# Optimization experiments

Hardware: AMD Instinct MI355X
Metric: run time of the kernel (lower is better)

## Reference

```python
import jax, jax.numpy as jnp
import numpy as np

N_NODES = 50000
N_EDGES = 800000
D = 64  # out_dim


def setup_inputs() -> dict:
    key = jax.random.key(0)
    ks = jax.random.split(key, 9)
    K_h = jax.random.normal(ks[0], (N_NODES, D), dtype=jnp.float32)
    Q_h = jax.random.normal(ks[1], (N_NODES, D), dtype=jnp.float32)
    P_e = jax.random.normal(ks[2], (N_NODES, D), dtype=jnp.float32)
    src = jax.random.randint(ks[3], (N_EDGES,), 0, N_NODES, dtype=jnp.int32)
    dst = jax.random.randint(ks[4], (N_EDGES,), 0, N_NODES, dtype=jnp.int32)
    # MLP params: Linear(D, D) -> ReLU -> Linear(D, 1)
    lim1 = 1.0 / np.sqrt(D)
    W1 = jax.random.uniform(ks[5], (D, D), minval=-lim1, maxval=lim1, dtype=jnp.float32)
    b1 = jax.random.uniform(ks[6], (D,), minval=-lim1, maxval=lim1, dtype=jnp.float32)
    W2 = jax.random.uniform(ks[7], (D, 1), minval=-lim1, maxval=lim1, dtype=jnp.float32)
    b2 = jax.random.uniform(ks[8], (1,), minval=-lim1, maxval=lim1, dtype=jnp.float32)
    return {"K_h": K_h, "Q_h": Q_h, "P_e": P_e, "src": src, "dst": dst,
            "W1": W1, "b1": b1, "W2": W2, "b2": b2}


def reference(K_h, Q_h, P_e, src, dst, W1, b1, W2, b2):
    # Per-edge gather: src node K_h and P_e, dst node Q_h -> [E, D]
    dif = K_h[src] - Q_h[dst] + P_e[src]
    # Tiny 2-layer MLP per edge: [E, D] -> [E, D] -> [E, 1]
    h = jax.nn.relu(dif @ W1 + b1)
    score = h @ W2 + b2  # [E, 1]
    return score
```

## Files before the change

### kernel.cpp

```cpp
#include <hip/hip_runtime.h>
#include <hip/hip_fp16.h>

#define DD 64
#define NPB 64
#define LP 72

typedef _Float16 f16x8 __attribute__((ext_vector_type(8)));
typedef float    f32x4 __attribute__((ext_vector_type(4)));

__global__ __launch_bounds__(256) void node_transform_mfma(
    const float* __restrict__ K_h, const float* __restrict__ Q_h,
    const float* __restrict__ P_e, const float* __restrict__ W1,
    const float* __restrict__ b1, __half* __restrict__ A,
    __half* __restrict__ Bm, int n_nodes)
{
    __shared__ __half XH [NPB][LP];
    __shared__ __half QH [NPB][LP];
    __shared__ __half W1T[DD][LP];

    const int tid   = threadIdx.x;
    const int nbase = blockIdx.x * NPB;

    {
        const int k  = tid >> 2;
        const int n0 = (tid & 3) << 4;
        const float* wr = W1 + k * DD + n0;
        float4 w0 = *(const float4*)(wr);
        float4 w1v = *(const float4*)(wr + 4);
        float4 w2v = *(const float4*)(wr + 8);
        float4 w3v = *(const float4*)(wr + 12);
        const float wv[16] = {w0.x,w0.y,w0.z,w0.w, w1v.x,w1v.y,w1v.z,w1v.w,
                              w2v.x,w2v.y,w2v.z,w2v.w, w3v.x,w3v.y,w3v.z,w3v.w};
#pragma unroll
        for (int j = 0; j < 16; ++j)
            W1T[n0 + j][k] = __float2half(wv[j]);
    }

#pragma unroll
    for (int ch = 0; ch < 4; ++ch) {
        int idx = tid + (ch << 8);
        int r   = idx >> 4;
        int q4  = idx & 15;
        int node = nbase + r;
        float4 kv = make_float4(0.f,0.f,0.f,0.f);
        float4 pv = kv, qv = kv;
        if (node < n_nodes) {
            kv = *(const float4*)(K_h + (size_t)node * DD + q4 * 4);
            pv = *(const float4*)(P_e + (size_t)node * DD + q4 * 4);
            qv = *(const float4*)(Q_h + (size_t)node * DD + q4 * 4);
        }
        __half2* xh = (__half2*)&XH[r][q4 << 2];
        xh[0] = __float22half2_rn(make_float2(kv.x + pv.x, kv.y + pv.y));
        xh[1] = __float22half2_rn(make_float2(kv.z + pv.z, kv.w + pv.w));
        __half2* qh = (__half2*)&QH[r][q4 << 2];
        qh[0] = __float22half2_rn(make_float2(qv.x, qv.y));
        qh[1] = __float22half2_rn(make_float2(qv.z, qv.w));
    }
    __syncthreads();

    const int w    = tid >> 6;
    const int lane = tid & 63;
    const int m    = lane & 15;
    const int q    = lane >> 4;
    const int row  = (w << 4) + m;

    f16x8 xlo = *(const f16x8*)&XH[row][(q << 3)];
    f16x8 xhi = *(const f16x8*)&XH[row][32 + (q << 3)];
    f16x8 qlo = *(const f16x8*)&QH[row][(q << 3)];
    f16x8 qhi = *(const f16x8*)&QH[row][32 + (q << 3)];

    f32x4 accA[4], accB[4];
#pragma unroll
    for (int t = 0; t < 4; ++t) {
        float bb = b1[t * 16 + m];
        accA[t] = (f32x4){bb, bb, bb, bb};
        accB[t] = (f32x4){0.f, 0.f, 0.f, 0.f};
        f16x8 wlo = *(const f16x8*)&W1T[t * 16 + m][(q << 3)];
        f16x8 whi = *(const f16x8*)&W1T[t * 16 + m][32 + (q << 3)];
        accA[t] = __builtin_amdgcn_mfma_f32_16x16x32_f16(xlo, wlo, accA[t], 0, 0, 0);
        accA[t] = __builtin_amdgcn_mfma_f32_16x16x32_f16(xhi, whi, accA[t], 0, 0, 0);
        accB[t] = __builtin_amdgcn_mfma_f32_16x16x32_f16(qlo, wlo, accB[t], 0, 0, 0);
        accB[t] = __builtin_amdgcn_mfma_f32_16x16x32_f16(qhi, whi, accB[t], 0, 0, 0);
    }

#pragma unroll
    for (int r = 0; r < 4; ++r) {
        int node = nbase + (w << 4) + (q << 2) + r;
        if (node >= n_nodes) continue;
        __half* Arow = A  + (size_t)node * DD + m;
        __half* Brow = Bm + (size_t)node * DD + m;
#pragma unroll
        for (int t = 0; t < 4; ++t) {
            Arow[t * 16] = __float2half(accA[t][r]);
            Brow[t * 16] = __float2half(accB[t][r]);
        }
    }
}

__global__ __launch_bounds__(256) void edge_score_kernel(
    const __half* __restrict__ A, const __half* __restrict__ Bm,
    const int* __restrict__ src, const int* __restrict__ dst,
    const float* __restrict__ W2, const float* __restrict__ b2,
    float* __restrict__ out, int n_edges)
{
    const int tid = threadIdx.x;
    const int g   = tid >> 3;
    const int c   = tid & 7;
    const int e0  = (blockIdx.x << 7) + (g << 2);
    if (e0 >= n_edges) return;

    float4 w0 = *(const float4*)(W2 + c * 8);
    float4 w1 = *(const float4*)(W2 + c * 8 + 4);
    const float wv[8] = {w0.x, w0.y, w0.z, w0.w, w1.x, w1.y, w1.z, w1.w};
    const size_t coff = (size_t)(c * 8);

    if (e0 + 3 < n_edges) {
        int4 sv = *(const int4*)(src + e0);
        int4 dv = *(const int4*)(dst + e0);

        float4 ra0 = *(const float4*)(A  + (size_t)sv.x * DD + coff);
        float4 rb0 = *(const float4*)(Bm + (size_t)dv.x * DD + coff);
        float4 ra1 = *(const float4*)(A  + (size_t)sv.y * DD + coff);
        float4 rb1 = *(const float4*)(Bm + (size_t)dv.y * DD + coff);
        float4 ra2 = *(const float4*)(A  + (size_t)sv.z * DD + coff);
        float4 rb2 = *(const float4*)(Bm + (size_t)dv.z * DD + coff);
        float4 ra3 = *(const float4*)(A  + (size_t)sv.w * DD + coff);
        float4 rb3 = *(const float4*)(Bm + (size_t)dv.w * DD + coff);

        float acc0 = 0.f, acc1 = 0.f, acc2 = 0.f, acc3 = 0.f;
        const __half2* ah0 = (const __half2*)&ra0;
        const __half2* bh0 = (const __half2*)&rb0;
        const __half2* ah1 = (const __half2*)&ra1;
        const __half2* bh1 = (const __half2*)&rb1;
        const __half2* ah2 = (const __half2*)&ra2;
        const __half2* bh2 = (const __half2*)&rb2;
        const __half2* ah3 = (const __half2*)&ra3;
        const __half2* bh3 = (const __half2*)&rb3;
#pragma unroll
        for (int j = 0; j < 4; ++j) {
            float2 x, y;
            x = __half22float2(ah0[j]); y = __half22float2(bh0[j]);
            acc0 = fmaf(fmaxf(x.x - y.x, 0.f), wv[2 * j + 0], acc0);
            acc0 = fmaf(fmaxf(x.y - y.y, 0.f), wv[2 * j + 1], acc0);
            x = __half22float2(ah1[j]); y = __half22float2(bh1[j]);
            acc1 = fmaf(fmaxf(x.x - y.x, 0.f), wv[2 * j + 0], acc1);
            acc1 = fmaf(fmaxf(x.y - y.y, 0.f), wv[2 * j + 1], acc1);
            x = __half22float2(ah2[j]); y = __half22float2(bh2[j]);
            acc2 = fmaf(fmaxf(x.x - y.x, 0.f), wv[2 * j + 0], acc2);
            acc2 = fmaf(fmaxf(x.y - y.y, 0.f), wv[2 * j + 1], acc2);
            x = __half22float2(ah3[j]); y = __half22float2(bh3[j]);
            acc3 = fmaf(fmaxf(x.x - y.x, 0.f), wv[2 * j + 0], acc3);
            acc3 = fmaf(fmaxf(x.y - y.y, 0.f), wv[2 * j + 1], acc3);
        }

        acc0 += __shfl_xor(acc0, 1); acc1 += __shfl_xor(acc1, 1);
        acc2 += __shfl_xor(acc2, 1); acc3 += __shfl_xor(acc3, 1);
        acc0 += __shfl_xor(acc0, 2); acc1 += __shfl_xor(acc1, 2);
        acc2 += __shfl_xor(acc2, 2); acc3 += __shfl_xor(acc3, 2);
        acc0 += __shfl_xor(acc0, 4); acc1 += __shfl_xor(acc1, 4);
        acc2 += __shfl_xor(acc2, 4); acc3 += __shfl_xor(acc3, 4);

        if (c == 0) {
            float bb = b2[0];
            *(float4*)(out + e0) =
                make_float4(acc0 + bb, acc1 + bb, acc2 + bb, acc3 + bb);
        }
    } else {
        for (int e = e0; e < n_edges && e < e0 + 4; ++e) {
            int s = src[e], d = dst[e];
            float4 ar = *(const float4*)(A  + (size_t)s * DD + coff);
            float4 br = *(const float4*)(Bm + (size_t)d * DD + coff);
            const __half2* ah = (const __half2*)&ar;
            const __half2* bh = (const __half2*)&br;
            float acc = 0.f;
#pragma unroll
            for (int j = 0; j < 4; ++j) {
                float2 x = __half22float2(ah[j]);
                float2 y = __half22float2(bh[j]);
                acc = fmaf(fmaxf(x.x - y.x, 0.f), wv[2 * j + 0], acc);
                acc = fmaf(fmaxf(x.y - y.y, 0.f), wv[2 * j + 1], acc);
            }
            acc += __shfl_xor(acc, 1);
            acc += __shfl_xor(acc, 2);
            acc += __shfl_xor(acc, 4);
            if (c == 0) out[e] = acc + b2[0];
        }
    }
}

extern "C" void kernel_launch(void* const* d_in, const int* in_sizes, int n_in,
                              void* d_out, int out_size, void* d_ws, size_t ws_size,
                              hipStream_t stream) {
    const float* K_h = (const float*)d_in[0];
    const float* Q_h = (const float*)d_in[1];
    const float* P_e = (const float*)d_in[2];
    const int*   src = (const int*)d_in[3];
    const int*   dst = (const int*)d_in[4];
    const float* W1  = (const float*)d_in[5];
    const float* b1  = (const float*)d_in[6];
    const float* W2  = (const float*)d_in[7];
    const float* b2  = (const float*)d_in[8];
    float* out = (float*)d_out;

    int n_nodes = in_sizes[0] / DD;
    int n_edges = in_sizes[3];

    __half* A  = (__half*)d_ws;
    __half* Bm = A + (size_t)n_nodes * DD;

    node_transform_mfma<<<(n_nodes + NPB - 1) / NPB, 256, 0, stream>>>(
        K_h, Q_h, P_e, W1, b1, A, Bm, n_nodes);
    edge_score_kernel<<<(n_edges + 127) / 128, 256, 0, stream>>>(
        A, Bm, src, dst, W2, b2, out, n_edges);
}
```

Before: 120.9 us.

## Bin edges by source node range before gathering to improve locality

Adds a histogram, scan and scatter pass that groups edges into coarse bins by src node index, then runs the edge scoring kernel over the reordered (src,dst) pairs and scatters each result back to its original edge slot. The aim is to make the A-row gathers hit nearby memory so they get more cache reuse. In exchange it adds three extra kernel launches, an extra pass over the src/dst arrays with shared-memory atomics, and an uncoalesced scatter of the output. The binning is rebuilt from scratch on every call.

```diff
diff --git a/kernel.cpp b/kernel.cpp
--- a/kernel.cpp
+++ b/kernel.cpp
@@ -4,6 +4,7 @@
 #define DD 64
 #define NPB 64
 #define LP 72
+#define MAXB 512
 
 typedef _Float16 f16x8 __attribute__((ext_vector_type(8)));
 typedef float    f32x4 __attribute__((ext_vector_type(4)));
@@ -12,7 +13,7 @@
     const float* __restrict__ K_h, const float* __restrict__ Q_h,
     const float* __restrict__ P_e, const float* __restrict__ W1,
     const float* __restrict__ b1, __half* __restrict__ A,
-    __half* __restrict__ Bm, int n_nodes)
+    __half* __restrict__ Bm, int n_nodes, int* __restrict__ counts)
 {
     __shared__ __half XH [NPB][LP];
     __shared__ __half QH [NPB][LP];
@@ -20,6 +21,10 @@
 
     const int tid   = threadIdx.x;
     const int nbase = blockIdx.x * NPB;
+
+    if (blockIdx.x == 0) {
+        for (int i = tid; i < MAXB; i += 256) counts[i] = 0;
+    }
 
     {
         const int k  = tid >> 2;
@@ -97,9 +102,78 @@
     }
 }
 
-__global__ __launch_bounds__(256) void edge_score_kernel(
+
+__global__ __launch_bounds__(256) void hist_kernel(
+    const int* __restrict__ src, int* __restrict__ counts,
+    int n_edges, int shift)
+{
+    __shared__ int lh[MAXB];
+    for (int i = threadIdx.x; i < MAXB; i += 256) lh[i] = 0;
+    __syncthreads();
+    int idx    = blockIdx.x * blockDim.x + threadIdx.x;
+    int stride = gridDim.x * blockDim.x;
+    for (int e = idx; e < n_edges; e += stride)
+        atomicAdd(&lh[src[e] >> shift], 1);
+    __syncthreads();
+    for (int i = threadIdx.x; i < MAXB; i += 256)
+        if (lh[i]) atomicAdd(&counts[i], lh[i]);
+}
+
+__global__ __launch_bounds__(MAXB) void scan_kernel(
+    const int* __restrict__ counts, int* __restrict__ cursors, int nb)
+{
+    __shared__ int buf[2][MAXB];
+    const int t = threadIdx.x;
+    int v = (t < nb) ? counts[t] : 0;
+    buf[0][t] = v;
+    __syncthreads();
+    int s = 0;
+#pragma unroll
+    for (int off = 1; off < MAXB; off <<= 1) {
+        int x = buf[s][t];
+        if (t >= off) x += buf[s][t - off];
+        buf[s ^ 1][t] = x;
+        s ^= 1;
+        __syncthreads();
+    }
+    if (t < nb) cursors[t] = buf[s][t] - v;
+}
+
+__global__ __launch_bounds__(256) void scatter_kernel(
+    const int* __restrict__ src, const int* __restrict__ dst,
+    int* __restrict__ cursors, int2* __restrict__ sd, int* __restrict__ eid,
+    int n_edges, int shift)
+{
+    __shared__ int lh[MAXB];
+    __shared__ int base[MAXB];
+    const int t     = threadIdx.x;
+    const int chunk = (n_edges + gridDim.x - 1) / gridDim.x;
+    const int e0    = blockIdx.x * chunk;
+    const int e1    = (e0 + chunk < n_edges) ? e0 + chunk : n_edges;
+
+    for (int i = t; i < MAXB; i += 256) lh[i] = 0;
+    __syncthreads();
+    for (int e = e0 + t; e < e1; e += 256)
+        atomicAdd(&lh[src[e] >> shift], 1);
+    __syncthreads();
+    for (int i = t; i < MAXB; i += 256) {
+        int c = lh[i];
+        base[i] = c ? atomicAdd(&cursors[i], c) : 0;
+        lh[i] = 0;
+    }
+    __syncthreads();
+    for (int e = e0 + t; e < e1; e += 256) {
+        int sv = src[e];
+        int b  = sv >> shift;
+        int pos = base[b] + atomicAdd(&lh[b], 1);
+        sd[pos]  = make_int2(sv, dst[e]);
+        eid[pos] = e;
+    }
+}
+
+__global__ __launch_bounds__(256) void edge_score_binned(
     const __half* __restrict__ A, const __half* __restrict__ Bm,
-    const int* __restrict__ src, const int* __restrict__ dst,
+    const int2* __restrict__ sd, const int* __restrict__ eid,
     const float* __restrict__ W2, const float* __restrict__ b2,
     float* __restrict__ out, int n_edges)
 {
@@ -115,17 +189,18 @@
     const size_t coff = (size_t)(c * 8);
 
     if (e0 + 3 < n_edges) {
-        int4 sv = *(const int4*)(src + e0);
-        int4 dv = *(const int4*)(dst + e0);
-
-        float4 ra0 = *(const float4*)(A  + (size_t)sv.x * DD + coff);
-        float4 rb0 = *(const float4*)(Bm + (size_t)dv.x * DD + coff);
-        float4 ra1 = *(const float4*)(A  + (size_t)sv.y * DD + coff);
-        float4 rb1 = *(const float4*)(Bm + (size_t)dv.y * DD + coff);
-        float4 ra2 = *(const float4*)(A  + (size_t)sv.z * DD + coff);
-        float4 rb2 = *(const float4*)(Bm + (size_t)dv.z * DD + coff);
-        float4 ra3 = *(const float4*)(A  + (size_t)sv.w * DD + coff);
-        float4 rb3 = *(const float4*)(Bm + (size_t)dv.w * DD + coff);
+        int4 p01 = *(const int4*)(sd + e0);
+        int4 p23 = *(const int4*)(sd + e0 + 2);
+        int4 ev  = *(const int4*)(eid + e0);
+
+        float4 ra0 = *(const float4*)(A  + (size_t)p01.x * DD + coff);
+        float4 rb0 = *(const float4*)(Bm + (size_t)p01.y * DD + coff);
+        float4 ra1 = *(const float4*)(A  + (size_t)p01.z * DD + coff);
+        float4 rb1 = *(const float4*)(Bm + (size_t)p01.w * DD + coff);
+        float4 ra2 = *(const float4*)(A  + (size_t)p23.x * DD + coff);
+        float4 rb2 = *(const float4*)(Bm + (size_t)p23.y * DD + coff);
+        float4 ra3 = *(const float4*)(A  + (size_t)p23.z * DD + coff);
+        float4 rb3 = *(const float4*)(Bm + (size_t)p23.w * DD + coff);
 
         float acc0 = 0.f, acc1 = 0.f, acc2 = 0.f, acc3 = 0.f;
         const __half2* ah0 = (const __half2*)&ra0;
@@ -162,14 +237,16 @@
 
         if (c == 0) {
             float bb = b2[0];
-            *(float4*)(out + e0) =
-                make_float4(acc0 + bb, acc1 + bb, acc2 + bb, acc3 + bb);
+            out[ev.x] = acc0 + bb;
+            out[ev.y] = acc1 + bb;
+            out[ev.z] = acc2 + bb;
+            out[ev.w] = acc3 + bb;
         }
     } else {
         for (int e = e0; e < n_edges && e < e0 + 4; ++e) {
-            int s = src[e], d = dst[e];
-            float4 ar = *(const float4*)(A  + (size_t)s * DD + coff);
-            float4 br = *(const float4*)(Bm + (size_t)d * DD + coff);
+            int2 p = sd[e];
+            float4 ar = *(const float4*)(A  + (size_t)p.x * DD + coff);
+            float4 br = *(const float4*)(Bm + (size_t)p.y * DD + coff);
             const __half2* ah = (const __half2*)&ar;
             const __half2* bh = (const __half2*)&br;
             float acc = 0.f;
@@ -183,7 +260,7 @@
             acc += __shfl_xor(acc, 1);
             acc += __shfl_xor(acc, 2);
             acc += __shfl_xor(acc, 4);
-            if (c == 0) out[e] = acc + b2[0];
+            if (c == 0) out[eid[e]] = acc + b2[0];
         }
     }
 }
@@ -205,11 +282,28 @@
     int n_nodes = in_sizes[0] / DD;
     int n_edges = in_sizes[3];
 
+    int shift = 7;
+    while ((((n_nodes - 1) >> shift) + 1) > MAXB) ++shift;
+    int nb = ((n_nodes - 1) >> shift) + 1;
+
+    size_t nA = (size_t)n_nodes * DD;
     __half* A  = (__half*)d_ws;
-    __half* Bm = A + (size_t)n_nodes * DD;
+    __half* Bm = A + nA;
+    char* p = (char*)(Bm + nA);
+    p = (char*)(((size_t)p + 255) & ~(size_t)255);
+    int2* sd = (int2*)p;   p += (size_t)n_edges * sizeof(int2);
+    p = (char*)(((size_t)p + 255) & ~(size_t)255);
+    int* eid = (int*)p;    p += (size_t)n_edges * sizeof(int);
+    p = (char*)(((size_t)p + 255) & ~(size_t)255);
+    int* counts  = (int*)p;  p += MAXB * sizeof(int);
+    int* cursors = (int*)p;
 
     node_transform_mfma<<<(n_nodes + NPB - 1) / NPB, 256, 0, stream>>>(
-        K_h, Q_h, P_e, W1, b1, A, Bm, n_nodes);
-    edge_score_kernel<<<(n_edges + 127) / 128, 256, 0, stream>>>(
-        A, Bm, src, dst, W2, b2, out, n_edges);
-}
+        K_h, Q_h, P_e, W1, b1, A, Bm, n_nodes, counts);
+    hist_kernel<<<256, 256, 0, stream>>>(src, counts, n_edges, shift);
+    scan_kernel<<<1, MAXB, 0, stream>>>(counts, cursors, nb);
+    scatter_kernel<<<256, 256, 0, stream>>>(src, dst, cursors, sd, eid,
+                                            n_edges, shift);
+    edge_score_binned<<<(n_edges + 127) / 128, 256, 0, stream>>>(
+        A, Bm, sd, eid, W2, b2, out, n_edges);
+}
```

New measurement: 162.9 us. +34.7%, slower.

## Use grid-stride persistent edge loop with index prefetch and nontemporal loads/stores

Applied to the files above, without the earlier changes.

The edge kernel becomes a grid-stride loop capped at 2048 blocks. Each group of 8 threads prefetches the next iteration's src/dst index quad while it gathers and reduces the current one. Index loads and output stores use nontemporal builtins so the streamed data does not pollute cache that the gathered A/B rows need. This trades fewer, longer-lived blocks for some loss of latency hiding from oversubscription, and moves tail handling to a single group.

```diff
diff --git a/kernel.cpp b/kernel.cpp
--- a/kernel.cpp
+++ b/kernel.cpp
@@ -7,6 +7,8 @@
 
 typedef _Float16 f16x8 __attribute__((ext_vector_type(8)));
 typedef float    f32x4 __attribute__((ext_vector_type(4)));
+typedef int      i32x4 __attribute__((ext_vector_type(4)));
+typedef float    fv4   __attribute__((ext_vector_type(4)));
 
 __global__ __launch_bounds__(256) void node_transform_mfma(
     const float* __restrict__ K_h, const float* __restrict__ Q_h,
@@ -106,67 +108,86 @@
     const int tid = threadIdx.x;
     const int g   = tid >> 3;
     const int c   = tid & 7;
-    const int e0  = (blockIdx.x << 7) + (g << 2);
-    if (e0 >= n_edges) return;
+    const int nq  = n_edges >> 2;
+    const int tg  = gridDim.x << 5;
 
     float4 w0 = *(const float4*)(W2 + c * 8);
     float4 w1 = *(const float4*)(W2 + c * 8 + 4);
     const float wv[8] = {w0.x, w0.y, w0.z, w0.w, w1.x, w1.y, w1.z, w1.w};
     const size_t coff = (size_t)(c * 8);
-
-    if (e0 + 3 < n_edges) {
-        int4 sv = *(const int4*)(src + e0);
-        int4 dv = *(const int4*)(dst + e0);
-
-        float4 ra0 = *(const float4*)(A  + (size_t)sv.x * DD + coff);
-        float4 rb0 = *(const float4*)(Bm + (size_t)dv.x * DD + coff);
-        float4 ra1 = *(const float4*)(A  + (size_t)sv.y * DD + coff);
-        float4 rb1 = *(const float4*)(Bm + (size_t)dv.y * DD + coff);
-        float4 ra2 = *(const float4*)(A  + (size_t)sv.z * DD + coff);
-        float4 rb2 = *(const float4*)(Bm + (size_t)dv.z * DD + coff);
-        float4 ra3 = *(const float4*)(A  + (size_t)sv.w * DD + coff);
-        float4 rb3 = *(const float4*)(Bm + (size_t)dv.w * DD + coff);
-
-        float acc0 = 0.f, acc1 = 0.f, acc2 = 0.f, acc3 = 0.f;
-        const __half2* ah0 = (const __half2*)&ra0;
-        const __half2* bh0 = (const __half2*)&rb0;
-        const __half2* ah1 = (const __half2*)&ra1;
-        const __half2* bh1 = (const __half2*)&rb1;
-        const __half2* ah2 = (const __half2*)&ra2;
-        const __half2* bh2 = (const __half2*)&rb2;
-        const __half2* ah3 = (const __half2*)&ra3;
-        const __half2* bh3 = (const __half2*)&rb3;
-#pragma unroll
-        for (int j = 0; j < 4; ++j) {
-            float2 x, y;
-            x = __half22float2(ah0[j]); y = __half22float2(bh0[j]);
-            acc0 = fmaf(fmaxf(x.x - y.x, 0.f), wv[2 * j + 0], acc0);
-            acc0 = fmaf(fmaxf(x.y - y.y, 0.f), wv[2 * j + 1], acc0);
-            x = __half22float2(ah1[j]); y = __half22float2(bh1[j]);
-            acc1 = fmaf(fmaxf(x.x - y.x, 0.f), wv[2 * j + 0], acc1);
-            acc1 = fmaf(fmaxf(x.y - y.y, 0.f), wv[2 * j + 1], acc1);
-            x = __half22float2(ah2[j]); y = __half22float2(bh2[j]);
-            acc2 = fmaf(fmaxf(x.x - y.x, 0.f), wv[2 * j + 0], acc2);
-            acc2 = fmaf(fmaxf(x.y - y.y, 0.f), wv[2 * j + 1], acc2);
-            x = __half22float2(ah3[j]); y = __half22float2(bh3[j]);
-            acc3 = fmaf(fmaxf(x.x - y.x, 0.f), wv[2 * j + 0], acc3);
-            acc3 = fmaf(fmaxf(x.y - y.y, 0.f), wv[2 * j + 1], acc3);
-        }
-
-        acc0 += __shfl_xor(acc0, 1); acc1 += __shfl_xor(acc1, 1);
-        acc2 += __shfl_xor(acc2, 1); acc3 += __shfl_xor(acc3, 1);
-        acc0 += __shfl_xor(acc0, 2); acc1 += __shfl_xor(acc1, 2);
-        acc2 += __shfl_xor(acc2, 2); acc3 += __shfl_xor(acc3, 2);
-        acc0 += __shfl_xor(acc0, 4); acc1 += __shfl_xor(acc1, 4);
-        acc2 += __shfl_xor(acc2, 4); acc3 += __shfl_xor(acc3, 4);
-
-        if (c == 0) {
-            float bb = b2[0];
-            *(float4*)(out + e0) =
-                make_float4(acc0 + bb, acc1 + bb, acc2 + bb, acc3 + bb);
-        }
-    } else {
-        for (int e = e0; e < n_edges && e < e0 + 4; ++e) {
+    const float bb = b2[0];
+
+    int q = (blockIdx.x << 5) + g;
+    if (q < nq) {
+        i32x4 sv = __builtin_nontemporal_load((const i32x4*)(src + (q << 2)));
+        i32x4 dv = __builtin_nontemporal_load((const i32x4*)(dst + (q << 2)));
+        for (;;) {
+            const int e0 = q << 2;
+            const int qn = q + tg;
+            const bool more = (qn < nq);
+            i32x4 svn, dvn;
+            if (more) {
+                svn = __builtin_nontemporal_load((const i32x4*)(src + (qn << 2)));
+                dvn = __builtin_nontemporal_load((const i32x4*)(dst + (qn << 2)));
+            }
+
+            float4 ra0 = *(const float4*)(A  + (size_t)sv[0] * DD + coff);
+            float4 rb0 = *(const float4*)(Bm + (size_t)dv[0] * DD + coff);
+            float4 ra1 = *(const float4*)(A  + (size_t)sv[1] * DD + coff);
+            float4 rb1 = *(const float4*)(Bm + (size_t)dv[1] * DD + coff);
+            float4 ra2 = *(const float4*)(A  + (size_t)sv[2] * DD + coff);
+            float4 rb2 = *(const float4*)(Bm + (size_t)dv[2] * DD + coff);
+            float4 ra3 = *(const float4*)(A  + (size_t)sv[3] * DD + coff);
+            float4 rb3 = *(const float4*)(Bm + (size_t)dv[3] * DD + coff);
+
+            float acc0 = 0.f, acc1 = 0.f, acc2 = 0.f, acc3 = 0.f;
+            const __half2* ah0 = (const __half2*)&ra0;
+            const __half2* bh0 = (const __half2*)&rb0;
+            const __half2* ah1 = (const __half2*)&ra1;
+            const __half2* bh1 = (const __half2*)&rb1;
+            const __half2* ah2 = (const __half2*)&ra2;
+            const __half2* bh2 = (const __half2*)&rb2;
+            const __half2* ah3 = (const __half2*)&ra3;
+            const __half2* bh3 = (const __half2*)&rb3;
+#pragma unroll
+            for (int j = 0; j < 4; ++j) {
+                float2 x, y;
+                x = __half22float2(ah0[j]); y = __half22float2(bh0[j]);
+                acc0 = fmaf(fmaxf(x.x - y.x, 0.f), wv[2 * j + 0], acc0);
+                acc0 = fmaf(fmaxf(x.y - y.y, 0.f), wv[2 * j + 1], acc0);
+                x = __half22float2(ah1[j]); y = __half22float2(bh1[j]);
+                acc1 = fmaf(fmaxf(x.x - y.x, 0.f), wv[2 * j + 0], acc1);
+                acc1 = fmaf(fmaxf(x.y - y.y, 0.f), wv[2 * j + 1], acc1);
+                x = __half22float2(ah2[j]); y = __half22float2(bh2[j]);
+                acc2 = fmaf(fmaxf(x.x - y.x, 0.f), wv[2 * j + 0], acc2);
+                acc2 = fmaf(fmaxf(x.y - y.y, 0.f), wv[2 * j + 1], acc2);
+                x = __half22float2(ah3[j]); y = __half22float2(bh3[j]);
+                acc3 = fmaf(fmaxf(x.x - y.x, 0.f), wv[2 * j + 0], acc3);
+                acc3 = fmaf(fmaxf(x.y - y.y, 0.f), wv[2 * j + 1], acc3);
+            }
+
+            acc0 += __shfl_xor(acc0, 1); acc1 += __shfl_xor(acc1, 1);
+            acc2 += __shfl_xor(acc2, 1); acc3 += __shfl_xor(acc3, 1);
+            acc0 += __shfl_xor(acc0, 2); acc1 += __shfl_xor(acc1, 2);
+            acc2 += __shfl_xor(acc2, 2); acc3 += __shfl_xor(acc3, 2);
+            acc0 += __shfl_xor(acc0, 4); acc1 += __shfl_xor(acc1, 4);
+            acc2 += __shfl_xor(acc2, 4); acc3 += __shfl_xor(acc3, 4);
+
+            if (c == 0) {
+                fv4 r;
+                r[0] = acc0 + bb; r[1] = acc1 + bb;
+                r[2] = acc2 + bb; r[3] = acc3 + bb;
+                __builtin_nontemporal_store(r, (fv4*)(out + e0));
+            }
+
+            if (!more) break;
+            q = qn; sv = svn; dv = dvn;
+        }
+    }
+
+    const int rem = n_edges & 3;
+    if (rem && blockIdx.x == 0 && g == 0) {
+        for (int e = n_edges - rem; e < n_edges; ++e) {
             int s = src[e], d = dst[e];
             float4 ar = *(const float4*)(A  + (size_t)s * DD + coff);
             float4 br = *(const float4*)(Bm + (size_t)d * DD + coff);
@@ -183,7 +204,7 @@
             acc += __shfl_xor(acc, 1);
             acc += __shfl_xor(acc, 2);
             acc += __shfl_xor(acc, 4);
-            if (c == 0) out[e] = acc + b2[0];
+            if (c == 0) out[e] = acc + bb;
         }
     }
 }
@@ -210,6 +231,11 @@
 
     node_transform_mfma<<<(n_nodes + NPB - 1) / NPB, 256, 0, stream>>>(
         K_h, Q_h, P_e, W1, b1, A, Bm, n_nodes);
-    edge_score_kernel<<<(n_edges + 127) / 128, 256, 0, stream>>>(
+
+    int nq = n_edges >> 2;
+    int grid = (nq + 31) >> 5;
+    if (grid > 2048) grid = 2048;
+    if (grid < 1) grid = 1;
+    edge_score_kernel<<<grid, 256, 0, stream>>>(
         A, Bm, src, dst, W2, b2, out, n_edges);
 }
```

Measured after the change: 120.6 us, median of 2. About the same (-0.3%).
